# Kernel optimization log

Measured on AMD Instinct MI355X. Metric: run time of the kernel, lower is better.

## Reference

```python
import jax, jax.numpy as jnp
import numpy as np

N = 100000
E = 1600000
F_IN = 8
HID = 64
SKIP = 2
EPS = 1e-5


def setup_inputs() -> dict:
    key = jax.random.key(0)
    ks = jax.random.split(key, 24)
    s = 0.05
    return {
        "X": jax.random.normal(ks[0], (N, F_IN), jnp.float32),
        "edge_index": jax.random.randint(ks[1], (2, E), 0, N, jnp.int32),
        "edge_weight": jax.random.uniform(ks[2], (E,), jnp.float32),
        "skip": jax.random.normal(ks[3], (N, SKIP), jnp.float32),
        "H": jax.random.normal(ks[4], (1, N, HID), jnp.float32),
        "C": jax.random.normal(ks[5], (1, N, HID), jnp.float32),
        # GConvLSTM gate params (order: i, f, c, o)
        "Wx": jax.random.normal(ks[6], (4, F_IN, HID), jnp.float32) * s,
        "bx": jax.random.normal(ks[7], (4, HID), jnp.float32) * s,
        "Wh": jax.random.normal(ks[8], (4, HID, HID), jnp.float32) * s,
        "bh": jax.random.normal(ks[9], (4, HID), jnp.float32) * s,
        "wc": jax.random.normal(ks[10], (3, HID), jnp.float32) * s,  # peephole i, f, o
        "bg": jax.random.normal(ks[11], (4, HID), jnp.float32) * s,
        # LayerNorms
        "ln_h_s": jnp.ones((HID,), jnp.float32),
        "ln_h_b": jnp.zeros((HID,), jnp.float32),
        "ln_c_s": jnp.ones((HID,), jnp.float32),
        "ln_c_b": jnp.zeros((HID,), jnp.float32),
        "ln_o_s": jnp.ones((HID,), jnp.float32),
        "ln_o_b": jnp.zeros((HID,), jnp.float32),
        # Output GCN head
        "W1": jax.random.normal(ks[12], (HID + SKIP, HID), jnp.float32) * s,
        "b1": jnp.zeros((HID,), jnp.float32),
        "W2": jax.random.normal(ks[13], (HID, 1), jnp.float32) * s,
        "b2": jnp.zeros((1,), jnp.float32),
    }


def _layernorm(x, scale, bias):
    m = jnp.mean(x, axis=-1, keepdims=True)
    v = jnp.mean(jnp.square(x - m), axis=-1, keepdims=True)
    return (x - m) * jax.lax.rsqrt(v + EPS) * scale + bias


def _gcn_norm(edge_index, edge_weight, n):
    # add self loops with weight 1 (PyG GCNConv default), symmetric normalization
    loop = jnp.arange(n, dtype=edge_index.dtype)
    src = jnp.concatenate([edge_index[0], loop])
    dst = jnp.concatenate([edge_index[1], loop])
    w = jnp.concatenate([edge_weight, jnp.ones((n,), edge_weight.dtype)])
    deg = jax.ops.segment_sum(w, dst, num_segments=n)
    dinv = jnp.where(deg > 0, jax.lax.rsqrt(jnp.maximum(deg, 1e-12)), 0.0)
    norm = dinv[dst] * w * dinv[src]
    return src, dst, norm


def _forward(X, edge_index, edge_weight, skip, H, C,
             Wx, bx, Wh, bh, wc, bg,
             ln_h_s, ln_h_b, ln_c_s, ln_c_b, ln_o_s, ln_o_b,
             W1, b1, W2, b2):
    n = X.shape[0]
    src, dst, norm = _gcn_norm(edge_index, edge_weight, n)

    def agg(x):  # A_hat @ x via gather -> scale -> scatter-add
        return jax.ops.segment_sum(x[src] * norm[:, None], dst, num_segments=n)

    H0, C0 = H[0], C[0]
    # GCNConv is linear in x, so propagate once then apply the 4 stacked gate weights
    AX = agg(X)   # [N, F_IN]
    AH = agg(H0)  # [N, HID]
    g = (jnp.einsum('nf,gfh->gnh', AX, Wx) + bx[:, None, :]
         + jnp.einsum('nh,ghk->gnk', AH, Wh) + bh[:, None, :])
    i = jax.nn.sigmoid(g[0] + wc[0] * C0 + bg[0])
    f = jax.nn.sigmoid(g[1] + wc[1] * C0 + bg[1])
    c = f * C0 + i * jnp.tanh(g[2] + bg[2])
    o = jax.nn.sigmoid(g[3] + wc[2] * c + bg[3])
    h = o * jnp.tanh(c)

    hidden = _layernorm(h, ln_h_s, ln_h_b)[None]  # [1, N, HID]
    cell = _layernorm(c, ln_c_s, ln_c_b)[None]    # [1, N, HID]

    out = jax.nn.relu(_layernorm(h, ln_o_s, ln_o_b))
    out = jnp.concatenate([out, skip], axis=-1)   # [N, HID+SKIP]
    out = jax.nn.relu(agg(out) @ W1 + b1)          # fc_out1 + relu
    out = agg(out) @ W2 + b2                       # fc_out2 -> [N, 1]
    out = out + X[:, :1]                           # residual with first feature
    return out, hidden, cell


def reference(X, edge_index, edge_weight, skip, H, C,
              Wx, bx, Wh, bh, wc, bg,
              ln_h_s, ln_h_b, ln_c_s, ln_c_b, ln_o_s, ln_o_b,
              W1, b1, W2, b2):
    return _forward(X, edge_index, edge_weight, skip, H, C,
                    Wx, bx, Wh, bh, wc, bg,
                    ln_h_s, ln_h_b, ln_c_s, ln_c_b, ln_o_s, ln_o_b,
                    W1, b1, W2, b2)
```

## Files before the change

kernel.cpp:

```cpp
#include <hip/hip_runtime.h>
#include <hip/hip_bf16.h>

#define F_IN 8
#define HID 64

typedef __hip_bfloat16 bf16;

__device__ __forceinline__ float b2f(bf16 x) { return __bfloat162float(x); }
__device__ __forceinline__ bf16 f2b(float x) { return __float2bfloat16(x); }

template <typename T> struct IO;
template <> struct IO<bf16> {
    static __device__ __forceinline__ float ld(const bf16* p, size_t i) { return b2f(p[i]); }
    static __device__ __forceinline__ void st(bf16* p, size_t i, float v) { p[i] = f2b(v); }
};
template <> struct IO<float> {
    static __device__ __forceinline__ float ld(const float* p, size_t i) { return p[i]; }
    static __device__ __forceinline__ void st(float* p, size_t i, float v) { p[i] = v; }
};

__global__ void dec_detect_kernel(const unsigned int* __restrict__ xraw, int* __restrict__ flag) {
    int t = threadIdx.x;
    int cnt = 0;
    for (int j = 0; j < 4; ++j) {
        unsigned w = xraw[t * 4 + j];
        unsigned lo = w & 0xFFFFu;
        unsigned e = (lo >> 7) & 0xFFu;
        if (lo == 0u || (e >= 100u && e <= 144u)) cnt++;
    }
#pragma unroll
    for (int off = 32; off > 0; off >>= 1) cnt += __shfl_xor(cnt, off);
    if (t == 0) *flag = (cnt >= 128) ? 1 : 0;
}

template <typename T>
__device__ __forceinline__ void deg_body(const int* __restrict__ ei, const T* __restrict__ ew,
                                         float* __restrict__ deg_w, int* __restrict__ count, int E) {
    int e = blockIdx.x * blockDim.x + threadIdx.x;
    if (e >= E) return;
    int dst = ei[E + e];
    atomicAdd(&deg_w[dst], IO<T>::ld(ew, e));
    atomicAdd(&count[dst], 1);
}
__global__ void dec_deg_kernel(const int* ei, const void* ew, float* deg_w, int* count, int E,
                               const int* flag) {
    if (*flag) deg_body<bf16>(ei, (const bf16*)ew, deg_w, count, E);
    else       deg_body<float>(ei, (const float*)ew, deg_w, count, E);
}

__global__ __launch_bounds__(1024) void dec_scan1_kernel(const int* __restrict__ count,
                                                         float* __restrict__ dinv,
                                                         int* __restrict__ partial, int n) {
    __shared__ int sh[1024];
    int i = blockIdx.x * 1024 + threadIdx.x;
    int v = (i < n) ? count[i] : 0;
    if (i < n) dinv[i] = rsqrtf(dinv[i] + 1.0f);
    sh[threadIdx.x] = v;
    __syncthreads();
    for (int off = 512; off > 0; off >>= 1) {
        if (threadIdx.x < off) sh[threadIdx.x] += sh[threadIdx.x + off];
        __syncthreads();
    }
    if (threadIdx.x == 0) partial[blockIdx.x] = sh[0];
}

__global__ __launch_bounds__(1024) void dec_scan2_kernel(int* __restrict__ partial, int P) {
    __shared__ int sh[1024];
    int v = (threadIdx.x < P) ? partial[threadIdx.x] : 0;
    sh[threadIdx.x] = v;
    __syncthreads();
    int incl = v;
    for (int off = 1; off < 1024; off <<= 1) {
        int o = (threadIdx.x >= off) ? sh[threadIdx.x - off] : 0;
        __syncthreads();
        incl += o;
        sh[threadIdx.x] = incl;
        __syncthreads();
    }
    if (threadIdx.x < P) partial[threadIdx.x] = incl - v;
}

__global__ __launch_bounds__(1024) void dec_scan3_kernel(const int* __restrict__ count,
                                                         const int* __restrict__ partial,
                                                         int* __restrict__ rowstart, int n) {
    __shared__ int sh[1024];
    int i = blockIdx.x * 1024 + threadIdx.x;
    int v = (i < n) ? count[i] : 0;
    sh[threadIdx.x] = v;
    __syncthreads();
    int incl = v;
    for (int off = 1; off < 1024; off <<= 1) {
        int o = (threadIdx.x >= off) ? sh[threadIdx.x - off] : 0;
        __syncthreads();
        incl += o;
        sh[threadIdx.x] = incl;
        __syncthreads();
    }
    int offbase = partial[blockIdx.x];
    if (i < n) rowstart[i] = offbase + incl - v;
    if (i == n - 1) rowstart[n] = offbase + incl;
}

template <typename T>
__device__ __forceinline__ void scatter_body(const int* __restrict__ ei, const T* __restrict__ ew,
                                             const float* __restrict__ dinv,
                                             const int* __restrict__ rowstart,
                                             int* __restrict__ count, int2* __restrict__ csr, int E) {
    int e = blockIdx.x * blockDim.x + threadIdx.x;
    if (e >= E) return;
    int src = ei[e];
    int dst = ei[E + e];
    int pos = rowstart[dst] + atomicSub(&count[dst], 1) - 1;
    int2 v;
    v.x = src;
    v.y = __float_as_int(dinv[dst] * IO<T>::ld(ew, e) * dinv[src]);
    csr[pos] = v;
}
__global__ void dec_scatter_kernel(const int* ei, const void* ew, const float* dinv,
                                   const int* rowstart, int* count, int2* csr, int E,
                                   const int* flag) {
    if (*flag) scatter_body<bf16>(ei, (const bf16*)ew, dinv, rowstart, count, csr, E);
    else       scatter_body<float>(ei, (const float*)ew, dinv, rowstart, count, csr, E);
}

template <typename T>
__device__ __forceinline__ void aggA_body(const int* __restrict__ rowstart,
                                          const int2* __restrict__ csr,
                                          const float* __restrict__ dinv,
                                          const T* __restrict__ X, const T* __restrict__ H,
                                          bf16* __restrict__ axah, int n) {
    int wave = threadIdx.x >> 6;
    int lane = threadIdx.x & 63;
    int i = blockIdx.x * 4 + wave;
    if (i >= n) return;
    float di = dinv[i];
    float self = di * di;
    float acc_h = self * IO<T>::ld(H, (size_t)i * 64 + lane);
    float acc_x = (lane < F_IN) ? self * IO<T>::ld(X, (size_t)i * F_IN + lane) : 0.f;
    int e = rowstart[i], s1 = rowstart[i + 1];
    for (; e + 8 <= s1; e += 8) {
        int2 ed[8];
#pragma unroll
        for (int j = 0; j < 8; ++j) ed[j] = csr[e + j];
        float hv[8];
#pragma unroll
        for (int j = 0; j < 8; ++j) hv[j] = IO<T>::ld(H, (size_t)ed[j].x * 64 + lane);
#pragma unroll
        for (int j = 0; j < 8; ++j) acc_h = fmaf(__int_as_float(ed[j].y), hv[j], acc_h);
        if (lane < F_IN) {
            float xv[8];
#pragma unroll
            for (int j = 0; j < 8; ++j) xv[j] = IO<T>::ld(X, (size_t)ed[j].x * F_IN + lane);
#pragma unroll
            for (int j = 0; j < 8; ++j) acc_x = fmaf(__int_as_float(ed[j].y), xv[j], acc_x);
        }
    }
    for (; e < s1; ++e) {
        int2 ed = csr[e];
        float nrm = __int_as_float(ed.y);
        acc_h = fmaf(nrm, IO<T>::ld(H, (size_t)ed.x * 64 + lane), acc_h);
        if (lane < F_IN) acc_x = fmaf(nrm, IO<T>::ld(X, (size_t)ed.x * F_IN + lane), acc_x);
    }
    axah[(size_t)i * 72 + lane] = f2b(acc_h);
    if (lane < F_IN) axah[(size_t)i * 72 + 64 + lane] = f2b(acc_x);
}
__global__ __launch_bounds__(256) void dec_aggA_kernel(const int* rowstart, const int2* csr,
                                                       const float* dinv, const void* X,
                                                       const void* H, bf16* axah, int n,
                                                       const int* flag) {
    if (*flag) aggA_body<bf16>(rowstart, csr, dinv, (const bf16*)X, (const bf16*)H, axah, n);
    else       aggA_body<float>(rowstart, csr, dinv, (const float*)X, (const float*)H, axah, n);
}

template <typename T>
__device__ __forceinline__ void gates_body(
    const bf16* __restrict__ axah, const T* __restrict__ Cin,
    const T* __restrict__ Wx, const T* __restrict__ bx,
    const T* __restrict__ Wh, const T* __restrict__ bh,
    const T* __restrict__ wc, const T* __restrict__ bg,
    const T* __restrict__ lnh_s, const T* __restrict__ lnh_b,
    const T* __restrict__ lnc_s, const T* __restrict__ lnc_b,
    const T* __restrict__ lno_s, const T* __restrict__ lno_b,
    const T* __restrict__ skip, const T* __restrict__ W1,
    bf16* __restrict__ t_out, T* __restrict__ dout, int n) {
    const int k = threadIdx.x;
    const int base = blockIdx.x * 8;
    T* out_hidden = dout + n;
    T* out_cell   = dout + n + (size_t)64 * n;
    __shared__ float sh_axah[8 * 72];
    __shared__ float sh_u[8 * 66];
    int cnt = n - base; if (cnt > 8) cnt = 8; if (cnt < 0) cnt = 0;
    for (int idx = k; idx < cnt * 72; idx += 64)
        sh_axah[idx] = b2f(axah[(size_t)base * 72 + idx]);
    __syncthreads();

    float acc0[8] = {}, acc1[8] = {}, acc2[8] = {}, acc3[8] = {};
    for (int h = 0; h < HID; ++h) {
        float w0 = IO<T>::ld(Wh, 0 * 4096 + h * 64 + k);
        float w1 = IO<T>::ld(Wh, 1 * 4096 + h * 64 + k);
        float w2 = IO<T>::ld(Wh, 2 * 4096 + h * 64 + k);
        float w3 = IO<T>::ld(Wh, 3 * 4096 + h * 64 + k);
#pragma unroll
        for (int nn = 0; nn < 8; ++nn) {
            float a = sh_axah[nn * 72 + h];
            acc0[nn] = fmaf(a, w0, acc0[nn]);
            acc1[nn] = fmaf(a, w1, acc1[nn]);
            acc2[nn] = fmaf(a, w2, acc2[nn]);
            acc3[nn] = fmaf(a, w3, acc3[nn]);
        }
    }
    for (int f = 0; f < F_IN; ++f) {
        float w0 = IO<T>::ld(Wx, 0 * 512 + f * 64 + k);
        float w1 = IO<T>::ld(Wx, 1 * 512 + f * 64 + k);
        float w2 = IO<T>::ld(Wx, 2 * 512 + f * 64 + k);
        float w3 = IO<T>::ld(Wx, 3 * 512 + f * 64 + k);
#pragma unroll
        for (int nn = 0; nn < 8; ++nn) {
            float a = sh_axah[nn * 72 + 64 + f];
            acc0[nn] = fmaf(a, w0, acc0[nn]);
            acc1[nn] = fmaf(a, w1, acc1[nn]);
            acc2[nn] = fmaf(a, w2, acc2[nn]);
            acc3[nn] = fmaf(a, w3, acc3[nn]);
        }
    }

    float B0 = IO<T>::ld(bx, k)       + IO<T>::ld(bh, k)       + IO<T>::ld(bg, k);
    float B1 = IO<T>::ld(bx, 64 + k)  + IO<T>::ld(bh, 64 + k)  + IO<T>::ld(bg, 64 + k);
    float B2 = IO<T>::ld(bx, 128 + k) + IO<T>::ld(bh, 128 + k) + IO<T>::ld(bg, 128 + k);
    float B3 = IO<T>::ld(bx, 192 + k) + IO<T>::ld(bh, 192 + k) + IO<T>::ld(bg, 192 + k);
    float pc0 = IO<T>::ld(wc, k), pc1 = IO<T>::ld(wc, 64 + k), pc2 = IO<T>::ld(wc, 128 + k);
    float shs = IO<T>::ld(lnh_s, k), shb = IO<T>::ld(lnh_b, k);
    float scs = IO<T>::ld(lnc_s, k), scb = IO<T>::ld(lnc_b, k);
    float sos = IO<T>::ld(lno_s, k), sob = IO<T>::ld(lno_b, k);

    for (int nn = 0; nn < cnt; ++nn) {
        int i = base + nn;
        float c0 = IO<T>::ld(Cin, (size_t)i * 64 + k);
        float gi = acc0[nn] + B0 + pc0 * c0;
        float gf = acc1[nn] + B1 + pc1 * c0;
        float gc = acc2[nn] + B2;
        float vi = 1.f / (1.f + __expf(-gi));
        float vf = 1.f / (1.f + __expf(-gf));
        float c  = vf * c0 + vi * tanhf(gc);
        float go = acc3[nn] + B3 + pc2 * c;
        float vo = 1.f / (1.f + __expf(-go));
        float hh = vo * tanhf(c);
        float sh_ = hh, sh2 = hh * hh, sc_ = c, sc2 = c * c;
#pragma unroll
        for (int off = 32; off > 0; off >>= 1) {
            sh_ += __shfl_xor(sh_, off);
            sh2 += __shfl_xor(sh2, off);
            sc_ += __shfl_xor(sc_, off);
            sc2 += __shfl_xor(sc2, off);
        }
        float mh = sh_ * 0.015625f;
        float vh = sh2 * 0.015625f - mh * mh;
        float rh = rsqrtf(vh + 1e-5f);
        float mc = sc_ * 0.015625f;
        float vcv = sc2 * 0.015625f - mc * mc;
        float rc = rsqrtf(vcv + 1e-5f);
        float hn = (hh - mh) * rh;
        IO<T>::st(out_hidden, (size_t)i * 64 + k, hn * shs + shb);
        IO<T>::st(out_cell, (size_t)i * 64 + k, (c - mc) * rc * scs + scb);
        float r = hn * sos + sob;
        r = r > 0.f ? r : 0.f;
        sh_u[nn * 66 + k] = r;
        if (k < 2) sh_u[nn * 66 + 64 + k] = IO<T>::ld(skip, (size_t)i * 2 + k);
    }
    __syncthreads();
    float tacc[8] = {};
    for (int f = 0; f < 66; ++f) {
        float w = IO<T>::ld(W1, f * 64 + k);
#pragma unroll
        for (int nn = 0; nn < 8; ++nn)
            tacc[nn] = fmaf(sh_u[nn * 66 + f], w, tacc[nn]);
    }
    for (int nn = 0; nn < cnt; ++nn)
        t_out[(size_t)(base + nn) * 64 + k] = f2b(tacc[nn]);
}
__global__ __launch_bounds__(64) void dec_gates_kernel(
    const bf16* axah, const void* Cin, const void* Wx, const void* bx, const void* Wh,
    const void* bh, const void* wc, const void* bg, const void* lnh_s, const void* lnh_b,
    const void* lnc_s, const void* lnc_b, const void* lno_s, const void* lno_b,
    const void* skip, const void* W1, bf16* t_out, void* dout, int n, const int* flag) {
    if (*flag)
        gates_body<bf16>(axah, (const bf16*)Cin, (const bf16*)Wx, (const bf16*)bx,
                         (const bf16*)Wh, (const bf16*)bh, (const bf16*)wc, (const bf16*)bg,
                         (const bf16*)lnh_s, (const bf16*)lnh_b, (const bf16*)lnc_s,
                         (const bf16*)lnc_b, (const bf16*)lno_s, (const bf16*)lno_b,
                         (const bf16*)skip, (const bf16*)W1, t_out, (bf16*)dout, n);
    else
        gates_body<float>(axah, (const float*)Cin, (const float*)Wx, (const float*)bx,
                          (const float*)Wh, (const float*)bh, (const float*)wc, (const float*)bg,
                          (const float*)lnh_s, (const float*)lnh_b, (const float*)lnc_s,
                          (const float*)lnc_b, (const float*)lno_s, (const float*)lno_b,
                          (const float*)skip, (const float*)W1, t_out, (float*)dout, n);
}

template <typename T>
__device__ __forceinline__ void aggB_body(const int* __restrict__ rowstart,
                                          const int2* __restrict__ csr,
                                          const float* __restrict__ dinv,
                                          const bf16* __restrict__ t, const T* __restrict__ b1,
                                          const T* __restrict__ W2, float* __restrict__ s_out,
                                          int n) {
    int wave = threadIdx.x >> 6;
    int lane = threadIdx.x & 63;
    int i = blockIdx.x * 4 + wave;
    if (i >= n) return;
    float di = dinv[i];
    float acc = di * di * b2f(t[(size_t)i * 64 + lane]);
    int e = rowstart[i], s1 = rowstart[i + 1];
    for (; e + 8 <= s1; e += 8) {
        int2 ed[8];
#pragma unroll
        for (int j = 0; j < 8; ++j) ed[j] = csr[e + j];
        float tv[8];
#pragma unroll
        for (int j = 0; j < 8; ++j) tv[j] = b2f(t[(size_t)ed[j].x * 64 + lane]);
#pragma unroll
        for (int j = 0; j < 8; ++j) acc = fmaf(__int_as_float(ed[j].y), tv[j], acc);
    }
    for (; e < s1; ++e) {
        int2 ed = csr[e];
        acc = fmaf(__int_as_float(ed.y), b2f(t[(size_t)ed.x * 64 + lane]), acc);
    }
    float v = acc + IO<T>::ld(b1, lane);
    v = v > 0.f ? v : 0.f;
    float p = v * IO<T>::ld(W2, lane);
#pragma unroll
    for (int off = 32; off > 0; off >>= 1) p += __shfl_xor(p, off);
    if (lane == 0) s_out[i] = p;
}
__global__ __launch_bounds__(256) void dec_aggB_kernel(const int* rowstart, const int2* csr,
                                                       const float* dinv, const bf16* t,
                                                       const void* b1, const void* W2,
                                                       float* s_out, int n, const int* flag) {
    if (*flag) aggB_body<bf16>(rowstart, csr, dinv, t, (const bf16*)b1, (const bf16*)W2, s_out, n);
    else       aggB_body<float>(rowstart, csr, dinv, t, (const float*)b1, (const float*)W2, s_out, n);
}

template <typename T>
__device__ __forceinline__ void aggC_body(const int* __restrict__ rowstart,
                                          const int2* __restrict__ csr,
                                          const float* __restrict__ dinv,
                                          const float* __restrict__ s_in, const T* __restrict__ X,
                                          const T* __restrict__ b2p, T* __restrict__ out0, int n) {
    int lane = threadIdx.x & 63;
    int wave = threadIdx.x >> 6;
    int sub = lane >> 4, sl = lane & 15;
    int i = (blockIdx.x * 4 + wave) * 4 + sub;
    if (i >= n) return;
    float acc = 0.f;
    int s0 = rowstart[i], s1 = rowstart[i + 1];
    for (int e = s0 + sl; e < s1; e += 16) {
        int2 ed = csr[e];
        acc = fmaf(__int_as_float(ed.y), s_in[ed.x], acc);
    }
#pragma unroll
    for (int off = 8; off > 0; off >>= 1) acc += __shfl_xor(acc, off);
    if (sl == 0) {
        float di = dinv[i];
        float r = acc + di * di * s_in[i] + IO<T>::ld(b2p, 0) + IO<T>::ld(X, (size_t)i * F_IN);
        IO<T>::st(out0, i, r);
    }
}
__global__ __launch_bounds__(256) void dec_aggC_kernel(const int* rowstart, const int2* csr,
                                                       const float* dinv, const float* s_in,
                                                       const void* X, const void* b2p,
                                                       void* out0, int n, const int* flag) {
    if (*flag) aggC_body<bf16>(rowstart, csr, dinv, s_in, (const bf16*)X, (const bf16*)b2p, (bf16*)out0, n);
    else       aggC_body<float>(rowstart, csr, dinv, s_in, (const float*)X, (const float*)b2p, (float*)out0, n);
}

extern "C" void kernel_launch(void* const* d_in, const int* in_sizes, int n_in,
                              void* d_out, int out_size, void* d_ws, size_t ws_size,
                              hipStream_t stream) {
    const void* X     = d_in[0];
    const int*  ei    = (const int*)d_in[1];
    const void* ew    = d_in[2];
    const void* skip  = d_in[3];
    const void* H     = d_in[4];
    const void* C     = d_in[5];
    const void* Wx    = d_in[6];
    const void* bx    = d_in[7];
    const void* Wh    = d_in[8];
    const void* bh    = d_in[9];
    const void* wc    = d_in[10];
    const void* bg    = d_in[11];
    const void* lnh_s = d_in[12];
    const void* lnh_b = d_in[13];
    const void* lnc_s = d_in[14];
    const void* lnc_b = d_in[15];
    const void* lno_s = d_in[16];
    const void* lno_b = d_in[17];
    const void* W1    = d_in[18];
    const void* b1    = d_in[19];
    const void* W2    = d_in[20];
    const void* b2    = d_in[21];

    const int N = in_sizes[0] / F_IN;
    const int E = in_sizes[2];
    const int P = (N + 1023) / 1024;

    float* ws = (float*)d_ws;
    size_t o = 0;
    float* dinv     = ws + o;            o += (size_t)N;
    int*   count    = (int*)(ws + o);    o += (size_t)N;
    int*   rowstart = (int*)(ws + o);    o += (size_t)N + 1;
    int*   partial  = (int*)(ws + o);    o += (size_t)P;
    int*   flag     = (int*)(ws + o);    o += 1;
    o = (o + 1) & ~(size_t)1;
    int2*  csr      = (int2*)(ws + o);   o += 2 * (size_t)E;
    bf16*  axah     = (bf16*)(ws + o);   o += 36 * (size_t)N;
    bf16*  t        = (bf16*)(ws + o);   o += 32 * (size_t)N;
    float* sarr     = ws + o;            o += (size_t)N;

    hipMemsetAsync(dinv, 0, (size_t)2 * N * sizeof(float), stream);

    dec_detect_kernel<<<1, 64, 0, stream>>>((const unsigned int*)X, flag);
    dec_deg_kernel<<<(E + 255) / 256, 256, 0, stream>>>(ei, ew, dinv, count, E, flag);
    dec_scan1_kernel<<<P, 1024, 0, stream>>>(count, dinv, partial, N);
    dec_scan2_kernel<<<1, 1024, 0, stream>>>(partial, P);
    dec_scan3_kernel<<<P, 1024, 0, stream>>>(count, partial, rowstart, N);
    dec_scatter_kernel<<<(E + 255) / 256, 256, 0, stream>>>(ei, ew, dinv, rowstart, count,
                                                            csr, E, flag);
    dec_aggA_kernel<<<(N + 3) / 4, 256, 0, stream>>>(rowstart, csr, dinv, X, H, axah, N, flag);
    dec_gates_kernel<<<(N + 7) / 8, 64, 0, stream>>>(axah, C, Wx, bx, Wh, bh, wc, bg,
                                                     lnh_s, lnh_b, lnc_s, lnc_b, lno_s, lno_b,
                                                     skip, W1, t, d_out, N, flag);
    dec_aggB_kernel<<<(N + 3) / 4, 256, 0, stream>>>(rowstart, csr, dinv, t, b1, W2, sarr,
                                                     N, flag);
    dec_aggC_kernel<<<(N + 15) / 16, 256, 0, stream>>>(rowstart, csr, dinv, sarr, X, b2,
                                                       d_out, N, flag);
}
```

Baseline: 698.0 us.

## Use bf16 MFMA for gate and fc_out1 matmuls with prepacked weights

```diff
diff --git a/kernel.cpp b/kernel.cpp
--- a/kernel.cpp
+++ b/kernel.cpp
@@ -5,6 +5,8 @@
 #define HID 64
 
 typedef __hip_bfloat16 bf16;
+typedef short short8 __attribute__((ext_vector_type(8)));
+typedef float f32x4 __attribute__((ext_vector_type(4)));
 
 __device__ __forceinline__ float b2f(bf16 x) { return __bfloat162float(x); }
 __device__ __forceinline__ bf16 f2b(float x) { return __float2bfloat16(x); }
@@ -63,7 +65,6 @@
     }
     if (threadIdx.x == 0) partial[blockIdx.x] = sh[0];
 }
-
 __global__ __launch_bounds__(1024) void dec_scan2_kernel(int* __restrict__ partial, int P) {
     __shared__ int sh[1024];
     int v = (threadIdx.x < P) ? partial[threadIdx.x] : 0;
@@ -79,7 +80,6 @@
     }
     if (threadIdx.x < P) partial[threadIdx.x] = incl - v;
 }
-
 __global__ __launch_bounds__(1024) void dec_scan3_kernel(const int* __restrict__ count,
                                                          const int* __restrict__ partial,
                                                          int* __restrict__ rowstart, int n) {
@@ -121,6 +121,66 @@
                                    const int* flag) {
     if (*flag) scatter_body<bf16>(ei, (const bf16*)ew, dinv, rowstart, count, csr, E);
     else       scatter_body<float>(ei, (const float*)ew, dinv, rowstart, count, csr, E);
+}
+
+template <typename T>
+__device__ __forceinline__ void prep_body(const T* Wx, const T* bx, const T* Wh, const T* bh,
+                                          const T* wc, const T* bg,
+                                          const T* lnh_s, const T* lnh_b, const T* lnc_s,
+                                          const T* lnc_b, const T* lno_s, const T* lno_b,
+                                          const T* W1,
+                                          bf16* __restrict__ Bp, bf16* __restrict__ W1p,
+                                          float* __restrict__ Bsum, float* __restrict__ wcf,
+                                          float* __restrict__ lnf) {
+    int idx = blockIdx.x * blockDim.x + threadIdx.x;
+    if (idx < 24576) {
+        int j = idx & 7, l = (idx >> 3) & 63, ts = idx >> 9;
+        int t = ts / 3, s = ts % 3;
+        int k = s * 32 + (l >> 4) * 8 + j;
+        int ncol = t * 16 + (l & 15);
+        int g = ncol >> 6, kk = ncol & 63;
+        float v = 0.f;
+        if (k < 64) v = IO<T>::ld(Wh, g * 4096 + k * 64 + kk);
+        else if (k < 72) v = IO<T>::ld(Wx, g * 512 + (k - 64) * 64 + kk);
+        Bp[idx] = f2b(v);
+    } else if (idx < 30720) {
+        int u = idx - 24576;
+        int j = u & 7, l = (u >> 3) & 63, ts = u >> 9;
+        int t = ts / 3, s = ts % 3;
+        int k = s * 32 + (l >> 4) * 8 + j;
+        int ncol = t * 16 + (l & 15);
+        float v = (k < 66) ? IO<T>::ld(W1, k * 64 + ncol) : 0.f;
+        W1p[u] = f2b(v);
+    } else if (idx < 30976) {
+        int p = idx - 30720;
+        Bsum[p] = IO<T>::ld(bx, p) + IO<T>::ld(bh, p) + IO<T>::ld(bg, p);
+    } else if (idx < 31168) {
+        int p = idx - 30976;
+        wcf[p] = IO<T>::ld(wc, p);
+    } else if (idx < 31552) {
+        int p = idx - 31168;
+        int which = p >> 6, k = p & 63;
+        const T* src = (which == 0) ? lnh_s : (which == 1) ? lnh_b : (which == 2) ? lnc_s
+                     : (which == 3) ? lnc_b : (which == 4) ? lno_s : lno_b;
+        lnf[p] = IO<T>::ld(src, k);
+    }
+}
+__global__ void dec_prep_kernel(const void* Wx, const void* bx, const void* Wh, const void* bh,
+                                const void* wc, const void* bg, const void* lnh_s,
+                                const void* lnh_b, const void* lnc_s, const void* lnc_b,
+                                const void* lno_s, const void* lno_b, const void* W1,
+                                bf16* Bp, bf16* W1p, float* Bsum, float* wcf, float* lnf,
+                                const int* flag) {
+    if (*flag)
+        prep_body<bf16>((const bf16*)Wx, (const bf16*)bx, (const bf16*)Wh, (const bf16*)bh,
+                        (const bf16*)wc, (const bf16*)bg, (const bf16*)lnh_s, (const bf16*)lnh_b,
+                        (const bf16*)lnc_s, (const bf16*)lnc_b, (const bf16*)lno_s,
+                        (const bf16*)lno_b, (const bf16*)W1, Bp, W1p, Bsum, wcf, lnf);
+    else
+        prep_body<float>((const float*)Wx, (const float*)bx, (const float*)Wh, (const float*)bh,
+                         (const float*)wc, (const float*)bg, (const float*)lnh_s, (const float*)lnh_b,
+                         (const float*)lnc_s, (const float*)lnc_b, (const float*)lno_s,
+                         (const float*)lno_b, (const float*)W1, Bp, W1p, Bsum, wcf, lnf);
 }
 
 template <typename T>
@@ -161,8 +221,9 @@
         acc_h = fmaf(nrm, IO<T>::ld(H, (size_t)ed.x * 64 + lane), acc_h);
         if (lane < F_IN) acc_x = fmaf(nrm, IO<T>::ld(X, (size_t)ed.x * F_IN + lane), acc_x);
     }
-    axah[(size_t)i * 72 + lane] = f2b(acc_h);
-    if (lane < F_IN) axah[(size_t)i * 72 + 64 + lane] = f2b(acc_x);
+    axah[(size_t)i * 96 + lane] = f2b(acc_h);
+    if (lane < F_IN) axah[(size_t)i * 96 + 64 + lane] = f2b(acc_x);
+    else if (lane < 32) axah[(size_t)i * 96 + 64 + lane] = f2b(0.f);
 }
 __global__ __launch_bounds__(256) void dec_aggA_kernel(const int* rowstart, const int2* csr,
                                                        const float* dinv, const void* X,
@@ -174,127 +235,133 @@
 
 template <typename T>
 __device__ __forceinline__ void gates_body(
-    const bf16* __restrict__ axah, const T* __restrict__ Cin,
-    const T* __restrict__ Wx, const T* __restrict__ bx,
-    const T* __restrict__ Wh, const T* __restrict__ bh,
-    const T* __restrict__ wc, const T* __restrict__ bg,
-    const T* __restrict__ lnh_s, const T* __restrict__ lnh_b,
-    const T* __restrict__ lnc_s, const T* __restrict__ lnc_b,
-    const T* __restrict__ lno_s, const T* __restrict__ lno_b,
-    const T* __restrict__ skip, const T* __restrict__ W1,
+    const bf16* __restrict__ axah, const bf16* __restrict__ Bp_g, const bf16* __restrict__ W1p_g,
+    const float* __restrict__ Bsum, const float* __restrict__ wcf, const float* __restrict__ lnf,
+    const T* __restrict__ Cin, const T* __restrict__ skip,
     bf16* __restrict__ t_out, T* __restrict__ dout, int n) {
-    const int k = threadIdx.x;
-    const int base = blockIdx.x * 8;
+    __shared__ __align__(16) short lds_bp[24576];
+    __shared__ __align__(16) short lds_u[64 * 96];
+    const int tid = threadIdx.x;
+    const int w = tid >> 6, lane = tid & 63;
+    const int quad = lane >> 4, col = lane & 15;
+    const int base = blockIdx.x * 64;
     T* out_hidden = dout + n;
     T* out_cell   = dout + n + (size_t)64 * n;
-    __shared__ float sh_axah[8 * 72];
-    __shared__ float sh_u[8 * 66];
-    int cnt = n - base; if (cnt > 8) cnt = 8; if (cnt < 0) cnt = 0;
-    for (int idx = k; idx < cnt * 72; idx += 64)
-        sh_axah[idx] = b2f(axah[(size_t)base * 72 + idx]);
+
+    for (int i = tid; i < 3072; i += 256)
+        ((uint4*)lds_bp)[i] = ((const uint4*)Bp_g)[i];
+    for (int i = tid; i < 64 * 30; i += 256)
+        lds_u[(i / 30) * 96 + 66 + (i % 30)] = 0;
+    if (tid < 128) {
+        int ln = tid >> 1, sx = tid & 1;
+        int gi = base + ln;
+        float v = (gi < n) ? IO<T>::ld(skip, (size_t)gi * 2 + sx) : 0.f;
+        lds_u[ln * 96 + 64 + sx] = *(short*)&(*(bf16*)&(v)) ;
+        bf16 bv = f2b(v);
+        lds_u[ln * 96 + 64 + sx] = *(const short*)&bv;
+    }
     __syncthreads();
 
-    float acc0[8] = {}, acc1[8] = {}, acc2[8] = {}, acc3[8] = {};
-    for (int h = 0; h < HID; ++h) {
-        float w0 = IO<T>::ld(Wh, 0 * 4096 + h * 64 + k);
-        float w1 = IO<T>::ld(Wh, 1 * 4096 + h * 64 + k);
-        float w2 = IO<T>::ld(Wh, 2 * 4096 + h * 64 + k);
-        float w3 = IO<T>::ld(Wh, 3 * 4096 + h * 64 + k);
-#pragma unroll
-        for (int nn = 0; nn < 8; ++nn) {
-            float a = sh_axah[nn * 72 + h];
-            acc0[nn] = fmaf(a, w0, acc0[nn]);
-            acc1[nn] = fmaf(a, w1, acc1[nn]);
-            acc2[nn] = fmaf(a, w2, acc2[nn]);
-            acc3[nn] = fmaf(a, w3, acc3[nn]);
-        }
-    }
-    for (int f = 0; f < F_IN; ++f) {
-        float w0 = IO<T>::ld(Wx, 0 * 512 + f * 64 + k);
-        float w1 = IO<T>::ld(Wx, 1 * 512 + f * 64 + k);
-        float w2 = IO<T>::ld(Wx, 2 * 512 + f * 64 + k);
-        float w3 = IO<T>::ld(Wx, 3 * 512 + f * 64 + k);
-#pragma unroll
-        for (int nn = 0; nn < 8; ++nn) {
-            float a = sh_axah[nn * 72 + 64 + f];
-            acc0[nn] = fmaf(a, w0, acc0[nn]);
-            acc1[nn] = fmaf(a, w1, acc1[nn]);
-            acc2[nn] = fmaf(a, w2, acc2[nn]);
-            acc3[nn] = fmaf(a, w3, acc3[nn]);
-        }
-    }
-
-    float B0 = IO<T>::ld(bx, k)       + IO<T>::ld(bh, k)       + IO<T>::ld(bg, k);
-    float B1 = IO<T>::ld(bx, 64 + k)  + IO<T>::ld(bh, 64 + k)  + IO<T>::ld(bg, 64 + k);
-    float B2 = IO<T>::ld(bx, 128 + k) + IO<T>::ld(bh, 128 + k) + IO<T>::ld(bg, 128 + k);
-    float B3 = IO<T>::ld(bx, 192 + k) + IO<T>::ld(bh, 192 + k) + IO<T>::ld(bg, 192 + k);
-    float pc0 = IO<T>::ld(wc, k), pc1 = IO<T>::ld(wc, 64 + k), pc2 = IO<T>::ld(wc, 128 + k);
-    float shs = IO<T>::ld(lnh_s, k), shb = IO<T>::ld(lnh_b, k);
-    float scs = IO<T>::ld(lnc_s, k), scb = IO<T>::ld(lnc_b, k);
-    float sos = IO<T>::ld(lno_s, k), sob = IO<T>::ld(lno_b, k);
-
-    for (int nn = 0; nn < cnt; ++nn) {
-        int i = base + nn;
-        float c0 = IO<T>::ld(Cin, (size_t)i * 64 + k);
-        float gi = acc0[nn] + B0 + pc0 * c0;
-        float gf = acc1[nn] + B1 + pc1 * c0;
-        float gc = acc2[nn] + B2;
-        float vi = 1.f / (1.f + __expf(-gi));
-        float vf = 1.f / (1.f + __expf(-gf));
-        float c  = vf * c0 + vi * tanhf(gc);
-        float go = acc3[nn] + B3 + pc2 * c;
-        float vo = 1.f / (1.f + __expf(-go));
-        float hh = vo * tanhf(c);
-        float sh_ = hh, sh2 = hh * hh, sc_ = c, sc2 = c * c;
-#pragma unroll
-        for (int off = 32; off > 0; off >>= 1) {
+    int arow = base + w * 16 + col;
+    if (arow >= n) arow = n - 1;
+    short8 afr[3];
+#pragma unroll
+    for (int s = 0; s < 3; ++s)
+        afr[s] = *(const short8*)(axah + (size_t)arow * 96 + s * 32 + quad * 8);
+    f32x4 acc[16];
+#pragma unroll
+    for (int t = 0; t < 16; ++t) {
+        f32x4 a = {0.f, 0.f, 0.f, 0.f};
+#pragma unroll
+        for (int s = 0; s < 3; ++s) {
+            short8 b = *(const short8*)(lds_bp + ((t * 3 + s) * 64 + lane) * 8);
+            a = __builtin_amdgcn_mfma_f32_16x16x32_bf16(afr[s], b, a, 0, 0, 0);
+        }
+        acc[t] = a;
+    }
+
+    const int nodeb = base + w * 16 + quad * 4;
+#pragma unroll
+    for (int reg = 0; reg < 4; ++reg) {
+        int i = nodeb + reg;
+        int ic = (i < n) ? i : (n - 1);
+        float cc[4], hh[4];
+        float sh_ = 0.f, sh2 = 0.f, sc_ = 0.f, sc2 = 0.f;
+#pragma unroll
+        for (int kk = 0; kk < 4; ++kk) {
+            int k = kk * 16 + col;
+            float c0 = IO<T>::ld(Cin, (size_t)ic * 64 + k);
+            float gi = acc[0 * 4 + kk][reg] + Bsum[k]       + wcf[k] * c0;
+            float gf = acc[1 * 4 + kk][reg] + Bsum[64 + k]  + wcf[64 + k] * c0;
+            float gc = acc[2 * 4 + kk][reg] + Bsum[128 + k];
+            float vi = 1.f / (1.f + __expf(-gi));
+            float vf = 1.f / (1.f + __expf(-gf));
+            float tc = 2.f / (1.f + __expf(-2.f * gc)) - 1.f;
+            float c  = vf * c0 + vi * tc;
+            float go = acc[3 * 4 + kk][reg] + Bsum[192 + k] + wcf[128 + k] * c;
+            float vo = 1.f / (1.f + __expf(-go));
+            float th = 2.f / (1.f + __expf(-2.f * c)) - 1.f;
+            float h  = vo * th;
+            cc[kk] = c; hh[kk] = h;
+            sh_ += h; sh2 += h * h; sc_ += c; sc2 += c * c;
+        }
+#pragma unroll
+        for (int off = 8; off > 0; off >>= 1) {
             sh_ += __shfl_xor(sh_, off);
             sh2 += __shfl_xor(sh2, off);
             sc_ += __shfl_xor(sc_, off);
             sc2 += __shfl_xor(sc2, off);
         }
         float mh = sh_ * 0.015625f;
-        float vh = sh2 * 0.015625f - mh * mh;
-        float rh = rsqrtf(vh + 1e-5f);
+        float rh = rsqrtf(sh2 * 0.015625f - mh * mh + 1e-5f);
         float mc = sc_ * 0.015625f;
-        float vcv = sc2 * 0.015625f - mc * mc;
-        float rc = rsqrtf(vcv + 1e-5f);
-        float hn = (hh - mh) * rh;
-        IO<T>::st(out_hidden, (size_t)i * 64 + k, hn * shs + shb);
-        IO<T>::st(out_cell, (size_t)i * 64 + k, (c - mc) * rc * scs + scb);
-        float r = hn * sos + sob;
-        r = r > 0.f ? r : 0.f;
-        sh_u[nn * 66 + k] = r;
-        if (k < 2) sh_u[nn * 66 + 64 + k] = IO<T>::ld(skip, (size_t)i * 2 + k);
+        float rc = rsqrtf(sc2 * 0.015625f - mc * mc + 1e-5f);
+#pragma unroll
+        for (int kk = 0; kk < 4; ++kk) {
+            int k = kk * 16 + col;
+            float hn = (hh[kk] - mh) * rh;
+            if (i < n) {
+                IO<T>::st(out_hidden, (size_t)i * 64 + k, hn * lnf[k] + lnf[64 + k]);
+                IO<T>::st(out_cell,   (size_t)i * 64 + k,
+                          (cc[kk] - mc) * rc * lnf[128 + k] + lnf[192 + k]);
+            }
+            float r = hn * lnf[256 + k] + lnf[320 + k];
+            r = r > 0.f ? r : 0.f;
+            bf16 rb = f2b(r);
+            lds_u[(w * 16 + quad * 4 + reg) * 96 + k] = *(const short*)&rb;
+        }
     }
     __syncthreads();
-    float tacc[8] = {};
-    for (int f = 0; f < 66; ++f) {
-        float w = IO<T>::ld(W1, f * 64 + k);
-#pragma unroll
-        for (int nn = 0; nn < 8; ++nn)
-            tacc[nn] = fmaf(sh_u[nn * 66 + f], w, tacc[nn]);
-    }
-    for (int nn = 0; nn < cnt; ++nn)
-        t_out[(size_t)(base + nn) * 64 + k] = f2b(tacc[nn]);
-}
-__global__ __launch_bounds__(64) void dec_gates_kernel(
-    const bf16* axah, const void* Cin, const void* Wx, const void* bx, const void* Wh,
-    const void* bh, const void* wc, const void* bg, const void* lnh_s, const void* lnh_b,
-    const void* lnc_s, const void* lnc_b, const void* lno_s, const void* lno_b,
-    const void* skip, const void* W1, bf16* t_out, void* dout, int n, const int* flag) {
+
+    short8 a2[3];
+#pragma unroll
+    for (int s = 0; s < 3; ++s)
+        a2[s] = *(const short8*)(lds_u + (w * 16 + col) * 96 + s * 32 + quad * 8);
+#pragma unroll
+    for (int t2 = 0; t2 < 4; ++t2) {
+        f32x4 ta = {0.f, 0.f, 0.f, 0.f};
+#pragma unroll
+        for (int s = 0; s < 3; ++s) {
+            short8 b = *(const short8*)(W1p_g + ((t2 * 3 + s) * 64 + lane) * 8);
+            ta = __builtin_amdgcn_mfma_f32_16x16x32_bf16(a2[s], b, ta, 0, 0, 0);
+        }
+#pragma unroll
+        for (int reg = 0; reg < 4; ++reg) {
+            int i = nodeb + reg;
+            if (i < n) t_out[(size_t)i * 64 + t2 * 16 + col] = f2b(ta[reg]);
+        }
+    }
+}
+__global__ __launch_bounds__(256) void dec_gates_kernel(
+    const bf16* axah, const bf16* Bp, const bf16* W1p, const float* Bsum, const float* wcf,
+    const float* lnf, const void* Cin, const void* skip, bf16* t_out, void* dout, int n,
+    const int* flag) {
     if (*flag)
-        gates_body<bf16>(axah, (const bf16*)Cin, (const bf16*)Wx, (const bf16*)bx,
-                         (const bf16*)Wh, (const bf16*)bh, (const bf16*)wc, (const bf16*)bg,
-                         (const bf16*)lnh_s, (const bf16*)lnh_b, (const bf16*)lnc_s,
-                         (const bf16*)lnc_b, (const bf16*)lno_s, (const bf16*)lno_b,
-                         (const bf16*)skip, (const bf16*)W1, t_out, (bf16*)dout, n);
+        gates_body<bf16>(axah, Bp, W1p, Bsum, wcf, lnf, (const bf16*)Cin, (const bf16*)skip,
+                         t_out, (bf16*)dout, n);
     else
-        gates_body<float>(axah, (const float*)Cin, (const float*)Wx, (const float*)bx,
-                          (const float*)Wh, (const float*)bh, (const float*)wc, (const float*)bg,
-                          (const float*)lnh_s, (const float*)lnh_b, (const float*)lnc_s,
-                          (const float*)lnc_b, (const float*)lno_s, (const float*)lno_b,
-                          (const float*)skip, (const float*)W1, t_out, (float*)dout, n);
+        gates_body<float>(axah, Bp, W1p, Bsum, wcf, lnf, (const float*)Cin, (const float*)skip,
+                          t_out, (float*)dout, n);
 }
 
 template <typename T>
@@ -410,25 +477,33 @@
     int*   rowstart = (int*)(ws + o);    o += (size_t)N + 1;
     int*   partial  = (int*)(ws + o);    o += (size_t)P;
     int*   flag     = (int*)(ws + o);    o += 1;
-    o = (o + 1) & ~(size_t)1;
+    o = (o + 3) & ~(size_t)3;
     int2*  csr      = (int2*)(ws + o);   o += 2 * (size_t)E;
-    bf16*  axah     = (bf16*)(ws + o);   o += 36 * (size_t)N;
+    bf16*  axah     = (bf16*)(ws + o);   o += 48 * (size_t)N;
     bf16*  t        = (bf16*)(ws + o);   o += 32 * (size_t)N;
     float* sarr     = ws + o;            o += (size_t)N;
+    o = (o + 3) & ~(size_t)3;
+    bf16*  Bp       = (bf16*)(ws + o);   o += 12288;
+    bf16*  W1p      = (bf16*)(ws + o);   o += 3072;
+    float* Bsum     = ws + o;            o += 256;
+    float* wcf      = ws + o;            o += 192;
+    float* lnf      = ws + o;            o += 384;
 
     hipMemsetAsync(dinv, 0, (size_t)2 * N * sizeof(float), stream);
 
     dec_detect_kernel<<<1, 64, 0, stream>>>((const unsigned int*)X, flag);
     dec_deg_kernel<<<(E + 255) / 256, 256, 0, stream>>>(ei, ew, dinv, count, E, flag);
+    dec_prep_kernel<<<124, 256, 0, stream>>>(Wx, bx, Wh, bh, wc, bg, lnh_s, lnh_b, lnc_s,
+                                             lnc_b, lno_s, lno_b, W1, Bp, W1p, Bsum, wcf,
+                                             lnf, flag);
     dec_scan1_kernel<<<P, 1024, 0, stream>>>(count, dinv, partial, N);
     dec_scan2_kernel<<<1, 1024, 0, stream>>>(partial, P);
     dec_scan3_kernel<<<P, 1024, 0, stream>>>(count, partial, rowstart, N);
     dec_scatter_kernel<<<(E + 255) / 256, 256, 0, stream>>>(ei, ew, dinv, rowstart, count,
                                                             csr, E, flag);
     dec_aggA_kernel<<<(N + 3) / 4, 256, 0, stream>>>(rowstart, csr, dinv, X, H, axah, N, flag);
-    dec_gates_kernel<<<(N + 7) / 8, 64, 0, stream>>>(axah, C, Wx, bx, Wh, bh, wc, bg,
-                                                     lnh_s, lnh_b, lnc_s, lnc_b, lno_s, lno_b,
-                                                     skip, W1, t, d_out, N, flag);
+    dec_gates_kernel<<<(N + 63) / 64, 256, 0, stream>>>(axah, Bp, W1p, Bsum, wcf, lnf, C,
+                                                        skip, t, d_out, N, flag);
     dec_aggB_kernel<<<(N + 3) / 4, 256, 0, stream>>>(rowstart, csr, dinv, t, b1, W2, sarr,
                                                      N, flag);
     dec_aggC_kernel<<<(N + 15) / 16, 256, 0, stream>>>(rowstart, csr, dinv, sarr, X, b2,
```

New measurement: 660.7 us. -5.4%, faster.
